# Performance work log

Measured on AMD Instinct MI355X. Metric: run time of the kernel, lower is better.

Reference implementation:

```python
import jax, jax.numpy as jnp
import numpy as np

N_HEAD = 8
DQK = 64
DV = 64
D_IN = 512
D_OUT = 512
D_MID = 2048
B = 4
L = 2048
EPS = 1e-5


def layernorm(x):
    mu = jnp.mean(x, axis=-1, keepdims=True)
    var = jnp.mean(jnp.square(x - mu), axis=-1, keepdims=True)
    return (x - mu) / jnp.sqrt(var + EPS)


def setup_inputs() -> dict:
    key = jax.random.key(0)
    ks = jax.random.split(key, 10)
    s = 0.02
    return {
        "query": jax.random.normal(ks[0], (B, L, D_IN), jnp.float32),
        "key": jax.random.normal(ks[1], (B, L, D_IN), jnp.float32),
        "value": jax.random.normal(ks[2], (B, L, D_IN), jnp.float32),
        "mask": jnp.zeros((B, L, L), jnp.float32),
        "WQ": jax.random.normal(ks[3], (D_IN, N_HEAD * DQK), jnp.float32) * s,
        "WK": jax.random.normal(ks[4], (D_IN, N_HEAD * DQK), jnp.float32) * s,
        "WV": jax.random.normal(ks[5], (D_IN, N_HEAD * DV), jnp.float32) * s,
        "WO": jax.random.normal(ks[6], (N_HEAD * DV, D_OUT), jnp.float32) * s,
        "W1": jax.random.normal(ks[7], (D_OUT, D_MID), jnp.float32) * s,
        "W2": jax.random.normal(ks[8], (D_MID, D_OUT), jnp.float32) * s,
    }


def reference(query, key, value, mask, WQ, WK, WV, WO, W1, W2):
    bsz = query.shape[0]
    # projections -> [b, h, l, d]
    Q = (query @ WQ).reshape(bsz, -1, N_HEAD, DQK).transpose(0, 2, 1, 3)
    K = (key @ WK).reshape(bsz, -1, N_HEAD, DQK).transpose(0, 2, 1, 3)
    V = (value @ WV).reshape(bsz, -1, N_HEAD, DV).transpose(0, 2, 1, 3)
    # scaled dot-product attention with additive mask [b, 1, lq, lk]
    scores = jnp.einsum("bhqd,bhkd->bhqk", Q, K) / jnp.sqrt(jnp.float32(DQK))
    w = jax.nn.softmax(scores + mask[:, None, :, :], axis=-1)
    out = jnp.einsum("bhqk,bhkd->bhqd", w, V)
    out = out.transpose(0, 2, 1, 3).reshape(bsz, -1, N_HEAD * DV)
    out = out @ WO
    out = layernorm(query + out)
    ff = jax.nn.relu(out @ W1) @ W2
    return layernorm(out + ff)
```

## Files before the change

### kernel.cpp

```cpp
#include <hip/hip_runtime.h>
#include <hip/hip_bf16.h>

using bf16 = __bf16;
typedef __bf16 bf16x4 __attribute__((ext_vector_type(4)));
typedef __bf16 bf16x8 __attribute__((ext_vector_type(8)));
typedef float f32x4 __attribute__((ext_vector_type(4)));

static constexpr int BATCH = 4;
static constexpr int SEQ   = 2048;
static constexpr int DIN   = 512;
static constexpr int NHEAD = 8;
static constexpr int DMID  = 2048;
static constexpr int MROWS = BATCH * SEQ;

__global__ __launch_bounds__(256) void mask_check(const uint4* __restrict__ m,
                                                  int* __restrict__ flag)
{
    const int base = (blockIdx.x * 256 + threadIdx.x) * 4;
    unsigned nz = 0;
    for (int i = 0; i < 4; ++i) {
        const uint4 v = m[base + i];
        nz |= v.x | v.y | v.z | v.w;
    }
    if (nz) atomicOr(flag, 1);
}

__global__ __launch_bounds__(256) void transpose_weights(
    const float* __restrict__ WQ, const float* __restrict__ WK,
    const float* __restrict__ WV, const float* __restrict__ WO,
    const float* __restrict__ W1, const float* __restrict__ W2,
    bf16* __restrict__ WQt, bf16* __restrict__ WKt, bf16* __restrict__ WVt,
    bf16* __restrict__ WOt, bf16* __restrict__ W1t, bf16* __restrict__ W2t)
{
    __shared__ float tile[32][33];
    const int bid = blockIdx.x;
    const float* in; bf16* out; int ip, op, cx, ry;
    if (bid < 1024) {
        const int w = bid >> 8, idx = bid & 255;
        in  = w == 0 ? WQ  : w == 1 ? WK  : w == 2 ? WV  : WO;
        out = w == 0 ? WQt : w == 1 ? WKt : w == 2 ? WVt : WOt;
        ip = 512; op = 512; cx = idx & 15; ry = idx >> 4;
    } else if (bid < 2048) {
        const int idx = bid - 1024;
        in = W1; out = W1t; ip = 2048; op = 512; cx = idx & 63; ry = idx >> 6;
    } else {
        const int idx = bid - 2048;
        in = W2; out = W2t; ip = 512; op = 2048; cx = idx & 15; ry = idx >> 4;
    }
    const int c0 = cx * 32, r0 = ry * 32;
    const int tx = threadIdx.x & 31, ty = threadIdx.x >> 5;
    for (int i = 0; i < 32; i += 8)
        tile[ty + i][tx] = in[(size_t)(r0 + ty + i) * ip + c0 + tx];
    __syncthreads();
    for (int i = 0; i < 32; i += 8)
        out[(size_t)(c0 + ty + i) * op + r0 + tx] = (bf16)tile[tx][ty + i];
}

__global__ __launch_bounds__(256) void transpose_b2b(const bf16* __restrict__ in,
                                                     bf16* __restrict__ out,
                                                     int ip, int op)
{
    __shared__ bf16 tile[32][33];
    const int c0 = blockIdx.x * 32;
    const int r0 = blockIdx.y * 32;
    const int tx = threadIdx.x & 31;
    const int ty = threadIdx.x >> 5;
    for (int i = 0; i < 32; i += 8)
        tile[ty + i][tx] = in[(size_t)(r0 + ty + i) * ip + c0 + tx];
    __syncthreads();
    for (int i = 0; i < 32; i += 8)
        out[(size_t)(c0 + ty + i) * op + r0 + tx] = tile[tx][ty + i];
}

template <int ACT>
__global__ __launch_bounds__(256) void gemm_skinny(const bf16* __restrict__ A,
                                                   const bf16* __restrict__ Bt,
                                                   bf16* __restrict__ C,
                                                   int M, int N, int K)
{
    __shared__ bf16 sA[32 * 72];
    __shared__ bf16 sB[256 * 72];

    const int t    = threadIdx.x;
    const int lane = t & 63;
    const int wave = t >> 6;
    const int wm   = wave >> 1;
    const int wn   = wave & 1;
    const int lr   = lane & 15;
    const int lq   = lane >> 4;

    const int m0 = blockIdx.y * 32;
    const int n0 = blockIdx.x * 256;

    const int ar = t >> 3;
    const int ac = (t & 7) * 8;

    f32x4 acc[8] = {};

    for (int k0 = 0; k0 < K; k0 += 64) {
        int4 av = *reinterpret_cast<const int4*>(A + (size_t)(m0 + ar) * K + k0 + ac);
        int4 bv[8];
        for (int i = 0; i < 8; ++i)
            bv[i] = *reinterpret_cast<const int4*>(Bt + (size_t)(n0 + i * 32 + ar) * K + k0 + ac);

        *reinterpret_cast<int4*>(&sA[ar * 72 + ac]) = av;
        for (int i = 0; i < 8; ++i)
            *reinterpret_cast<int4*>(&sB[(i * 32 + ar) * 72 + ac]) = bv[i];
        __syncthreads();

        for (int kk = 0; kk < 2; ++kk) {
            bf16x8 af = *reinterpret_cast<const bf16x8*>(&sA[(wm * 16 + lr) * 72 + kk * 32 + lq * 8]);
            for (int ni = 0; ni < 8; ++ni) {
                bf16x8 bfr = *reinterpret_cast<const bf16x8*>(&sB[(wn * 128 + ni * 16 + lr) * 72 + kk * 32 + lq * 8]);
                acc[ni] = __builtin_amdgcn_mfma_f32_16x16x32_bf16(af, bfr, acc[ni], 0, 0, 0);
            }
        }
        __syncthreads();
    }

    for (int ni = 0; ni < 8; ++ni) {
        const int col = n0 + wn * 128 + ni * 16 + lr;
        for (int j = 0; j < 4; ++j) {
            const int row = m0 + wm * 16 + lq * 4 + j;
            float v = acc[ni][j];
            if (ACT == 1) v = v > 0.f ? v : 0.f;
            C[(size_t)row * N + col] = (bf16)v;
        }
    }
}

__device__ inline int4 cvt16(const float* p)
{
    const float4 f0 = *reinterpret_cast<const float4*>(p);
    const float4 f1 = *reinterpret_cast<const float4*>(p + 4);
    bf16x8 r;
    r[0] = (bf16)f0.x; r[1] = (bf16)f0.y; r[2] = (bf16)f0.z; r[3] = (bf16)f0.w;
    r[4] = (bf16)f1.x; r[5] = (bf16)f1.y; r[6] = (bf16)f1.z; r[7] = (bf16)f1.w;
    return *reinterpret_cast<int4*>(&r);
}

__global__ __launch_bounds__(256) void gemm_qkv(const float* __restrict__ q,
                                                const float* __restrict__ k,
                                                const float* __restrict__ v,
                                                const bf16* __restrict__ WQt,
                                                const bf16* __restrict__ WKt,
                                                const bf16* __restrict__ WVt,
                                                bf16* __restrict__ Qb,
                                                bf16* __restrict__ Kb,
                                                bf16* __restrict__ Vb)
{
    const float* A  = blockIdx.z == 0 ? q   : blockIdx.z == 1 ? k   : v;
    const bf16*  Bt = blockIdx.z == 0 ? WQt : blockIdx.z == 1 ? WKt : WVt;
    bf16*        C  = blockIdx.z == 0 ? Qb  : blockIdx.z == 1 ? Kb  : Vb;
    const int K = DIN, N = DIN;

    __shared__ bf16 sA[32 * 72];
    __shared__ bf16 sB[256 * 72];

    const int t    = threadIdx.x;
    const int lane = t & 63;
    const int wave = t >> 6;
    const int wm   = wave >> 1;
    const int wn   = wave & 1;
    const int lr   = lane & 15;
    const int lq   = lane >> 4;

    const int m0 = blockIdx.y * 32;
    const int n0 = blockIdx.x * 256;

    const int ar = t >> 3;
    const int ac = (t & 7) * 8;

    f32x4 acc[8] = {};

    for (int k0 = 0; k0 < K; k0 += 64) {
        int4 av = cvt16(A + (size_t)(m0 + ar) * K + k0 + ac);
        int4 bv[8];
        for (int i = 0; i < 8; ++i)
            bv[i] = *reinterpret_cast<const int4*>(Bt + (size_t)(n0 + i * 32 + ar) * K + k0 + ac);

        *reinterpret_cast<int4*>(&sA[ar * 72 + ac]) = av;
        for (int i = 0; i < 8; ++i)
            *reinterpret_cast<int4*>(&sB[(i * 32 + ar) * 72 + ac]) = bv[i];
        __syncthreads();

        for (int kk = 0; kk < 2; ++kk) {
            bf16x8 af = *reinterpret_cast<const bf16x8*>(&sA[(wm * 16 + lr) * 72 + kk * 32 + lq * 8]);
            for (int ni = 0; ni < 8; ++ni) {
                bf16x8 bfr = *reinterpret_cast<const bf16x8*>(&sB[(wn * 128 + ni * 16 + lr) * 72 + kk * 32 + lq * 8]);
                acc[ni] = __builtin_amdgcn_mfma_f32_16x16x32_bf16(af, bfr, acc[ni], 0, 0, 0);
            }
        }
        __syncthreads();
    }

    for (int ni = 0; ni < 8; ++ni) {
        const int col = n0 + wn * 128 + ni * 16 + lr;
        for (int j = 0; j < 4; ++j) {
            const int row = m0 + wm * 16 + lq * 4 + j;
            C[(size_t)row * N + col] = (bf16)acc[ni][j];
        }
    }
}

__global__ __launch_bounds__(256) void attn_kernel(const bf16* __restrict__ Qb,
                                                   const bf16* __restrict__ Kb,
                                                   const bf16* __restrict__ Vt,
                                                   const float* __restrict__ mask,
                                                   bf16* __restrict__ O,
                                                   const int* __restrict__ mzf)
{
    const int bi   = blockIdx.x;
    const int xcd  = bi & 7;
    const int slot = bi >> 3;
    const int pair = xcd * 4 + (slot >> 5);
    const int qt   = slot & 31;
    const int h    = pair >> 2;
    const int b    = pair & 3;

    const int t    = threadIdx.x;
    const int lane = t & 63;
    const int wave = t >> 6;
    const int lr   = lane & 15;
    const int lq   = lane >> 4;
    const int q0   = qt * 64;
    const bool useM = (*mzf != 0);

    __shared__ bf16 sK[64 * 72];
    __shared__ bf16 sV[64 * 72];
    __shared__ bf16 sP[4][16 * 72];
    __shared__ bf16 sM[64 * 68];

    const int  qrow = q0 + wave * 16 + lr;
    const bf16* qp  = Qb + (size_t)(b * SEQ + qrow) * DIN + h * 64 + lq * 8;
    const bf16x8 qf0 = *reinterpret_cast<const bf16x8*>(qp);
    const bf16x8 qf1 = *reinterpret_cast<const bf16x8*>(qp + 32);

    f32x4 o[4] = {};
    f32x4 lrow = {};

    const int sr = t >> 2;
    const int sc = (t & 3) << 3;

    const bf16*  kbase = Kb + (size_t)(b * SEQ) * DIN + h * 64;
    const bf16*  vbase = Vt + (size_t)(h * 64 + sr) * MROWS + b * SEQ;
    const float* mbase = mask + ((size_t)b * SEQ + q0) * SEQ;

    constexpr float L2E = 1.4426950408889634f;
    constexpr float SCL = 0.125f * L2E;
    const bf16x8 ones = {(bf16)1.f, (bf16)1.f, (bf16)1.f, (bf16)1.f,
                         (bf16)1.f, (bf16)1.f, (bf16)1.f, (bf16)1.f};

    int4 kr0 = *reinterpret_cast<const int4*>(kbase + (size_t)sr * DIN + sc);
    int4 kr1 = *reinterpret_cast<const int4*>(kbase + (size_t)sr * DIN + sc + 32);
    int4 vr0 = *reinterpret_cast<const int4*>(vbase + sc);
    int4 vr1 = *reinterpret_cast<const int4*>(vbase + sc + 32);

    for (int tile = 0; tile < SEQ / 64; ++tile) {
        if (tile) __syncthreads();

        *reinterpret_cast<int4*>(&sK[sr * 72 + sc])      = kr0;
        *reinterpret_cast<int4*>(&sK[sr * 72 + sc + 32]) = kr1;
        *reinterpret_cast<int4*>(&sV[sr * 72 + sc])      = vr0;
        *reinterpret_cast<int4*>(&sV[sr * 72 + sc + 32]) = vr1;
        if (useM) {
            const int k0 = tile * 64;
            for (int i = 0; i < 4; ++i) {
                const int idx = t + 256 * i;
                const float4 mr = *reinterpret_cast<const float4*>(
                    mbase + (size_t)(idx >> 4) * SEQ + k0 + (idx & 15) * 4);
                bf16x4 mv;
                mv[0] = (bf16)(mr.x * L2E); mv[1] = (bf16)(mr.y * L2E);
                mv[2] = (bf16)(mr.z * L2E); mv[3] = (bf16)(mr.w * L2E);
                *reinterpret_cast<bf16x4*>(&sM[(idx >> 4) * 68 + (idx & 15) * 4]) = mv;
            }
        }

        if (tile + 1 < SEQ / 64) {
            const int k0 = (tile + 1) * 64;
            kr0 = *reinterpret_cast<const int4*>(kbase + (size_t)(k0 + sr) * DIN + sc);
            kr1 = *reinterpret_cast<const int4*>(kbase + (size_t)(k0 + sr) * DIN + sc + 32);
            vr0 = *reinterpret_cast<const int4*>(vbase + k0 + sc);
            vr1 = *reinterpret_cast<const int4*>(vbase + k0 + sc + 32);
        }
        __syncthreads();

        f32x4 sf[4] = {};
        for (int s = 0; s < 2; ++s) {
            const bf16x8 qf = s ? qf1 : qf0;
            for (int ni = 0; ni < 4; ++ni) {
                bf16x8 kf = *reinterpret_cast<const bf16x8*>(&sK[(ni * 16 + lr) * 72 + s * 32 + lq * 8]);
                sf[ni] = __builtin_amdgcn_mfma_f32_16x16x32_bf16(qf, kf, sf[ni], 0, 0, 0);
            }
        }

        if (useM) {
            for (int j = 0; j < 4; ++j) {
                const int mr2 = (wave * 16 + lq * 4 + j) * 68;
                for (int ni = 0; ni < 4; ++ni) {
                    const float mval = (float)sM[mr2 + ni * 16 + lr];
                    sP[wave][(lq * 4 + j) * 72 + ni * 16 + lr] = (bf16)exp2f(sf[ni][j] * SCL + mval);
                }
            }
        } else {
            for (int j = 0; j < 4; ++j)
                for (int ni = 0; ni < 4; ++ni)
                    sP[wave][(lq * 4 + j) * 72 + ni * 16 + lr] = (bf16)exp2f(sf[ni][j] * SCL);
        }

        f32x4 rs = {};
        for (int s = 0; s < 2; ++s) {
            bf16x8 pf = *reinterpret_cast<const bf16x8*>(&sP[wave][lr * 72 + s * 32 + lq * 8]);
            rs = __builtin_amdgcn_mfma_f32_16x16x32_bf16(pf, ones, rs, 0, 0, 0);
            for (int ni = 0; ni < 4; ++ni) {
                bf16x8 vf = *reinterpret_cast<const bf16x8*>(&sV[(ni * 16 + lr) * 72 + s * 32 + lq * 8]);
                o[ni] = __builtin_amdgcn_mfma_f32_16x16x32_bf16(pf, vf, o[ni], 0, 0, 0);
            }
        }
        for (int j = 0; j < 4; ++j)
            lrow[j] += rs[j];
    }

    for (int ni = 0; ni < 4; ++ni)
        for (int j = 0; j < 4; ++j) {
            const int row = q0 + wave * 16 + lq * 4 + j;
            const int col = h * 64 + ni * 16 + lr;
            O[(size_t)(b * SEQ + row) * DIN + col] = (bf16)(o[ni][j] / lrow[j]);
        }
}

__global__ __launch_bounds__(256) void add_ln(const float* __restrict__ X,
                                              const bf16* __restrict__ Y,
                                              bf16* __restrict__ Ob,
                                              float* __restrict__ Of)
{
    const int row  = blockIdx.x * 4 + (threadIdx.x >> 6);
    const int lane = threadIdx.x & 63;
    const size_t base = (size_t)row * DIN + lane * 8;
    const float4 x0 = *reinterpret_cast<const float4*>(X + base);
    const float4 x1 = *reinterpret_cast<const float4*>(X + base + 4);
    const bf16x8 yv = *reinterpret_cast<const bf16x8*>(Y + base);
    float v[8] = {x0.x, x0.y, x0.z, x0.w, x1.x, x1.y, x1.z, x1.w};
    float s = 0.f;
    for (int i = 0; i < 8; ++i) { v[i] += (float)yv[i]; s += v[i]; }
    for (int off = 1; off < 64; off <<= 1) s += __shfl_xor(s, off);
    const float mu = s * (1.f / DIN);
    float var = 0.f;
    for (int i = 0; i < 8; ++i) { const float d = v[i] - mu; var += d * d; }
    for (int off = 1; off < 64; off <<= 1) var += __shfl_xor(var, off);
    const float rstd = rsqrtf(var * (1.f / DIN) + 1e-5f);
    float r[8];
    for (int i = 0; i < 8; ++i) r[i] = (v[i] - mu) * rstd;
    if (Ob) {
        bf16x8 ov;
        for (int i = 0; i < 8; ++i) ov[i] = (bf16)r[i];
        *reinterpret_cast<bf16x8*>(Ob + base) = ov;
    }
    if (Of) {
        *reinterpret_cast<float4*>(Of + base)     = make_float4(r[0], r[1], r[2], r[3]);
        *reinterpret_cast<float4*>(Of + base + 4) = make_float4(r[4], r[5], r[6], r[7]);
    }
}

extern "C" void kernel_launch(void* const* d_in, const int* in_sizes, int n_in,
                              void* d_out, int out_size, void* d_ws, size_t ws_size,
                              hipStream_t stream)
{
    const float* query = (const float*)d_in[0];
    const float* key   = (const float*)d_in[1];
    const float* value = (const float*)d_in[2];
    const float* mask  = (const float*)d_in[3];
    const float* WQ    = (const float*)d_in[4];
    const float* WK    = (const float*)d_in[5];
    const float* WV    = (const float*)d_in[6];
    const float* WO    = (const float*)d_in[7];
    const float* W1    = (const float*)d_in[8];
    const float* W2    = (const float*)d_in[9];

    char* w = (char*)d_ws;
    size_t off = 0;
    auto carve2 = [&](size_t elems) { bf16* p = (bf16*)(w + off); off += elems * 2; return p; };
    auto carve4 = [&](size_t elems) { float* p = (float*)(w + off); off += elems * 4; return p; };

    bf16* Qb    = carve2((size_t)MROWS * DIN);
    bf16* Kb    = carve2((size_t)MROWS * DIN);
    bf16* Vb    = carve2((size_t)MROWS * DIN);
    bf16* Vt    = carve2((size_t)MROWS * DIN);
    bf16* Mid   = carve2((size_t)MROWS * DMID);
    float* Ln1f = carve4((size_t)MROWS * DIN);
    bf16* WQt   = carve2((size_t)DIN * DIN);
    bf16* WKt   = carve2((size_t)DIN * DIN);
    bf16* WVt   = carve2((size_t)DIN * DIN);
    bf16* WOt   = carve2((size_t)DIN * DIN);
    bf16* W1t   = carve2((size_t)DIN * DMID);
    bf16* W2t   = carve2((size_t)DMID * DIN);
    int*  mzf   = (int*)(w + off); off += 16;
    if (off > ws_size) return;

    bf16* Ob   = Vb;
    bf16* Two  = Qb;
    bf16* Ln1b = Kb;
    bf16* F2   = Vt;

    const dim3 blk(256);

    hipMemsetAsync(mzf, 0, 4, stream);
    mask_check<<<dim3(4096), blk, 0, stream>>>((const uint4*)mask, mzf);

    transpose_weights<<<dim3(3072), blk, 0, stream>>>(WQ, WK, WV, WO, W1, W2,
                                                      WQt, WKt, WVt, WOt, W1t, W2t);

    gemm_qkv<<<dim3(DIN / 256, MROWS / 32, 3), blk, 0, stream>>>(query, key, value,
                                                                 WQt, WKt, WVt, Qb, Kb, Vb);

    transpose_b2b<<<dim3(DIN / 32, MROWS / 32), blk, 0, stream>>>(Vb, Vt, DIN, MROWS);

    attn_kernel<<<dim3(1024), blk, 0, stream>>>(Qb, Kb, Vt, mask, Ob, mzf);

    gemm_skinny<0><<<dim3(DIN / 256, MROWS / 32), blk, 0, stream>>>(Ob, WOt, Two, MROWS, DIN, DIN);
    add_ln<<<dim3(MROWS / 4), blk, 0, stream>>>(query, Two, Ln1b, Ln1f);

    gemm_skinny<1><<<dim3(DMID / 256, MROWS / 32), blk, 0, stream>>>(Ln1b, W1t, Mid, MROWS, DMID, DIN);
    gemm_skinny<0><<<dim3(DIN / 256, MROWS / 32), blk, 0, stream>>>(Mid, W2t, F2, MROWS, DIN, DMID);

    add_ln<<<dim3(MROWS / 4), blk, 0, stream>>>(Ln1f, F2, (bf16*)nullptr, (float*)d_out);
}
```

Before: 393.9 us.

## Switch GEMMs to 128x128 tiles with direct global-to-LDS loads

Replaces the 32x256 skinny GEMM tiles with square 128x128 tiles. Each wave now computes a 4x4 grid of 16x16 MFMA outputs, which raises operand reuse from shared memory and cuts global traffic per FLOP. The bf16 operand loads use the global_load_lds builtin to write straight into LDS, bypassing registers. The fp32 QKV input path still converts through registers. The LDS rows lose their padding, which may add bank conflicts on fragment reads, and there is no double buffering.

```diff
diff --git a/kernel.cpp b/kernel.cpp
--- a/kernel.cpp
+++ b/kernel.cpp
@@ -12,6 +12,13 @@
 static constexpr int NHEAD = 8;
 static constexpr int DMID  = 2048;
 static constexpr int MROWS = BATCH * SEQ;
+
+__device__ __forceinline__ void gload16(const void* g, void* l)
+{
+    __builtin_amdgcn_global_load_lds(
+        (const __attribute__((address_space(1))) unsigned int*)g,
+        (__attribute__((address_space(3))) unsigned int*)l, 16, 0, 0);
+}
 
 __global__ __launch_bounds__(256) void mask_check(const uint4* __restrict__ m,
                                                   int* __restrict__ flag)
@@ -72,15 +79,13 @@
         out[(size_t)(c0 + ty + i) * op + r0 + tx] = tile[tx][ty + i];
 }
 
-template <int ACT>
-__global__ __launch_bounds__(256) void gemm_skinny(const bf16* __restrict__ A,
-                                                   const bf16* __restrict__ Bt,
-                                                   bf16* __restrict__ C,
-                                                   int M, int N, int K)
-{
-    __shared__ bf16 sA[32 * 72];
-    __shared__ bf16 sB[256 * 72];
-
+template <int ACT, bool AF32>
+__device__ __forceinline__ void gemm128_body(const void* __restrict__ Ain,
+                                             const bf16* __restrict__ Bt,
+                                             bf16* __restrict__ C,
+                                             int N, int K,
+                                             bf16* sA, bf16* sB)
+{
     const int t    = threadIdx.x;
     const int lane = t & 63;
     const int wave = t >> 6;
@@ -89,118 +94,111 @@
     const int lr   = lane & 15;
     const int lq   = lane >> 4;
 
-    const int m0 = blockIdx.y * 32;
-    const int n0 = blockIdx.x * 256;
-
-    const int ar = t >> 3;
-    const int ac = (t & 7) * 8;
-
-    f32x4 acc[8] = {};
+    const int m0 = blockIdx.y * 128;
+    const int n0 = blockIdx.x * 128;
+
+    const int srow = lane >> 3;
+    const int scol = (lane & 7) * 8;
+
+    f32x4 acc[4][4] = {};
 
     for (int k0 = 0; k0 < K; k0 += 64) {
-        int4 av = *reinterpret_cast<const int4*>(A + (size_t)(m0 + ar) * K + k0 + ac);
-        int4 bv[8];
-        for (int i = 0; i < 8; ++i)
-            bv[i] = *reinterpret_cast<const int4*>(Bt + (size_t)(n0 + i * 32 + ar) * K + k0 + ac);
-
-        *reinterpret_cast<int4*>(&sA[ar * 72 + ac]) = av;
-        for (int i = 0; i < 8; ++i)
-            *reinterpret_cast<int4*>(&sB[(i * 32 + ar) * 72 + ac]) = bv[i];
+        if constexpr (AF32) {
+            const float* Af = (const float*)Ain;
+            float4 fa[8];
+#pragma unroll
+            for (int i = 0; i < 4; ++i) {
+                const float* p = Af + (size_t)(m0 + (wave * 4 + i) * 8 + srow) * K + k0 + scol;
+                fa[2 * i]     = *reinterpret_cast<const float4*>(p);
+                fa[2 * i + 1] = *reinterpret_cast<const float4*>(p + 4);
+            }
+            if (k0) __syncthreads();
+#pragma unroll
+            for (int i = 0; i < 4; ++i) {
+                const int ch = wave * 4 + i;
+                gload16(Bt + (size_t)(n0 + ch * 8 + srow) * K + k0 + scol, sB + ch * 512);
+            }
+#pragma unroll
+            for (int i = 0; i < 4; ++i) {
+                const int r = (wave * 4 + i) * 8 + srow;
+                const float4 a = fa[2 * i], b = fa[2 * i + 1];
+                bf16x8 h;
+                h[0] = (bf16)a.x; h[1] = (bf16)a.y; h[2] = (bf16)a.z; h[3] = (bf16)a.w;
+                h[4] = (bf16)b.x; h[5] = (bf16)b.y; h[6] = (bf16)b.z; h[7] = (bf16)b.w;
+                *reinterpret_cast<bf16x8*>(&sA[r * 64 + scol]) = h;
+            }
+        } else {
+            const bf16* Ab = (const bf16*)Ain;
+            if (k0) __syncthreads();
+#pragma unroll
+            for (int i = 0; i < 4; ++i) {
+                const int ch = wave * 4 + i;
+                const int r  = ch * 8 + srow;
+                gload16(Ab + (size_t)(m0 + r) * K + k0 + scol, sA + ch * 512);
+                gload16(Bt + (size_t)(n0 + r) * K + k0 + scol, sB + ch * 512);
+            }
+        }
         __syncthreads();
 
+#pragma unroll
         for (int kk = 0; kk < 2; ++kk) {
-            bf16x8 af = *reinterpret_cast<const bf16x8*>(&sA[(wm * 16 + lr) * 72 + kk * 32 + lq * 8]);
-            for (int ni = 0; ni < 8; ++ni) {
-                bf16x8 bfr = *reinterpret_cast<const bf16x8*>(&sB[(wn * 128 + ni * 16 + lr) * 72 + kk * 32 + lq * 8]);
-                acc[ni] = __builtin_amdgcn_mfma_f32_16x16x32_bf16(af, bfr, acc[ni], 0, 0, 0);
-            }
-        }
-        __syncthreads();
-    }
-
-    for (int ni = 0; ni < 8; ++ni) {
-        const int col = n0 + wn * 128 + ni * 16 + lr;
-        for (int j = 0; j < 4; ++j) {
-            const int row = m0 + wm * 16 + lq * 4 + j;
-            float v = acc[ni][j];
-            if (ACT == 1) v = v > 0.f ? v : 0.f;
-            C[(size_t)row * N + col] = (bf16)v;
-        }
-    }
-}
-
-__device__ inline int4 cvt16(const float* p)
-{
-    const float4 f0 = *reinterpret_cast<const float4*>(p);
-    const float4 f1 = *reinterpret_cast<const float4*>(p + 4);
-    bf16x8 r;
-    r[0] = (bf16)f0.x; r[1] = (bf16)f0.y; r[2] = (bf16)f0.z; r[3] = (bf16)f0.w;
-    r[4] = (bf16)f1.x; r[5] = (bf16)f1.y; r[6] = (bf16)f1.z; r[7] = (bf16)f1.w;
-    return *reinterpret_cast<int4*>(&r);
-}
-
-__global__ __launch_bounds__(256) void gemm_qkv(const float* __restrict__ q,
-                                                const float* __restrict__ k,
-                                                const float* __restrict__ v,
-                                                const bf16* __restrict__ WQt,
-                                                const bf16* __restrict__ WKt,
-                                                const bf16* __restrict__ WVt,
-                                                bf16* __restrict__ Qb,
-                                                bf16* __restrict__ Kb,
-                                                bf16* __restrict__ Vb)
-{
-    const float* A  = blockIdx.z == 0 ? q   : blockIdx.z == 1 ? k   : v;
-    const bf16*  Bt = blockIdx.z == 0 ? WQt : blockIdx.z == 1 ? WKt : WVt;
-    bf16*        C  = blockIdx.z == 0 ? Qb  : blockIdx.z == 1 ? Kb  : Vb;
-    const int K = DIN, N = DIN;
-
-    __shared__ bf16 sA[32 * 72];
-    __shared__ bf16 sB[256 * 72];
-
-    const int t    = threadIdx.x;
-    const int lane = t & 63;
-    const int wave = t >> 6;
-    const int wm   = wave >> 1;
-    const int wn   = wave & 1;
-    const int lr   = lane & 15;
-    const int lq   = lane >> 4;
-
-    const int m0 = blockIdx.y * 32;
-    const int n0 = blockIdx.x * 256;
-
-    const int ar = t >> 3;
-    const int ac = (t & 7) * 8;
-
-    f32x4 acc[8] = {};
-
-    for (int k0 = 0; k0 < K; k0 += 64) {
-        int4 av = cvt16(A + (size_t)(m0 + ar) * K + k0 + ac);
-        int4 bv[8];
-        for (int i = 0; i < 8; ++i)
-            bv[i] = *reinterpret_cast<const int4*>(Bt + (size_t)(n0 + i * 32 + ar) * K + k0 + ac);
-
-        *reinterpret_cast<int4*>(&sA[ar * 72 + ac]) = av;
-        for (int i = 0; i < 8; ++i)
-            *reinterpret_cast<int4*>(&sB[(i * 32 + ar) * 72 + ac]) = bv[i];
-        __syncthreads();
-
-        for (int kk = 0; kk < 2; ++kk) {
-            bf16x8 af = *reinterpret_cast<const bf16x8*>(&sA[(wm * 16 + lr) * 72 + kk * 32 + lq * 8]);
-            for (int ni = 0; ni < 8; ++ni) {
-                bf16x8 bfr = *reinterpret_cast<const bf16x8*>(&sB[(wn * 128 + ni * 16 + lr) * 72 + kk * 32 + lq * 8]);
-                acc[ni] = __builtin_amdgcn_mfma_f32_16x16x32_bf16(af, bfr, acc[ni], 0, 0, 0);
-            }
-        }
-        __syncthreads();
-    }
-
-    for (int ni = 0; ni < 8; ++ni) {
-        const int col = n0 + wn * 128 + ni * 16 + lr;
-        for (int j = 0; j < 4; ++j) {
-            const int row = m0 + wm * 16 + lq * 4 + j;
-            C[(size_t)row * N + col] = (bf16)acc[ni][j];
-        }
-    }
+            bf16x8 af[4], bfr[4];
+#pragma unroll
+            for (int x = 0; x < 4; ++x) {
+                af[x]  = *reinterpret_cast<const bf16x8*>(&sA[(wm * 64 + x * 16 + lr) * 64 + kk * 32 + lq * 8]);
+                bfr[x] = *reinterpret_cast<const bf16x8*>(&sB[(wn * 64 + x * 16 + lr) * 64 + kk * 32 + lq * 8]);
+            }
+#pragma unroll
+            for (int m = 0; m < 4; ++m)
+#pragma unroll
+                for (int n = 0; n < 4; ++n)
+                    acc[m][n] = __builtin_amdgcn_mfma_f32_16x16x32_bf16(af[m], bfr[n], acc[m][n], 0, 0, 0);
+        }
+    }
+
+#pragma unroll
+    for (int n = 0; n < 4; ++n) {
+        const int col = n0 + wn * 64 + n * 16 + lr;
+#pragma unroll
+        for (int m = 0; m < 4; ++m) {
+            const int rowb = m0 + wm * 64 + m * 16 + lq * 4;
+#pragma unroll
+            for (int j = 0; j < 4; ++j) {
+                float v = acc[m][n][j];
+                if (ACT == 1) v = v > 0.f ? v : 0.f;
+                C[(size_t)(rowb + j) * N + col] = (bf16)v;
+            }
+        }
+    }
+}
+
+template <int ACT>
+__global__ __launch_bounds__(256) void gemm128(const bf16* __restrict__ A,
+                                               const bf16* __restrict__ Bt,
+                                               bf16* __restrict__ C,
+                                               int N, int K)
+{
+    __shared__ bf16 sA[128 * 64];
+    __shared__ bf16 sB[128 * 64];
+    gemm128_body<ACT, false>(A, Bt, C, N, K, sA, sB);
+}
+
+__global__ __launch_bounds__(256) void gemm128_qkv(const float* __restrict__ q,
+                                                   const float* __restrict__ k,
+                                                   const float* __restrict__ v,
+                                                   const bf16* __restrict__ WQt,
+                                                   const bf16* __restrict__ WKt,
+                                                   const bf16* __restrict__ WVt,
+                                                   bf16* __restrict__ Qb,
+                                                   bf16* __restrict__ Kb,
+                                                   bf16* __restrict__ Vb)
+{
+    __shared__ bf16 sA[128 * 64];
+    __shared__ bf16 sB[128 * 64];
+    const void* A  = blockIdx.z == 0 ? (const void*)q : blockIdx.z == 1 ? (const void*)k : (const void*)v;
+    const bf16* Bt = blockIdx.z == 0 ? WQt : blockIdx.z == 1 ? WKt : WVt;
+    bf16*       C  = blockIdx.z == 0 ? Qb  : blockIdx.z == 1 ? Kb  : Vb;
+    gemm128_body<0, true>(A, Bt, C, DIN, DIN, sA, sB);
 }
 
 __global__ __launch_bounds__(256) void attn_kernel(const bf16* __restrict__ Qb,
@@ -410,18 +408,18 @@
     transpose_weights<<<dim3(3072), blk, 0, stream>>>(WQ, WK, WV, WO, W1, W2,
                                                       WQt, WKt, WVt, WOt, W1t, W2t);
 
-    gemm_qkv<<<dim3(DIN / 256, MROWS / 32, 3), blk, 0, stream>>>(query, key, value,
-                                                                 WQt, WKt, WVt, Qb, Kb, Vb);
+    gemm128_qkv<<<dim3(DIN / 128, MROWS / 128, 3), blk, 0, stream>>>(query, key, value,
+                                                                     WQt, WKt, WVt, Qb, Kb, Vb);
 
     transpose_b2b<<<dim3(DIN / 32, MROWS / 32), blk, 0, stream>>>(Vb, Vt, DIN, MROWS);
 
     attn_kernel<<<dim3(1024), blk, 0, stream>>>(Qb, Kb, Vt, mask, Ob, mzf);
 
-    gemm_skinny<0><<<dim3(DIN / 256, MROWS / 32), blk, 0, stream>>>(Ob, WOt, Two, MROWS, DIN, DIN);
+    gemm128<0><<<dim3(DIN / 128, MROWS / 128), blk, 0, stream>>>(Ob, WOt, Two, DIN, DIN);
     add_ln<<<dim3(MROWS / 4), blk, 0, stream>>>(query, Two, Ln1b, Ln1f);
 
-    gemm_skinny<1><<<dim3(DMID / 256, MROWS / 32), blk, 0, stream>>>(Ln1b, W1t, Mid, MROWS, DMID, DIN);
-    gemm_skinny<0><<<dim3(DIN / 256, MROWS / 32), blk, 0, stream>>>(Mid, W2t, F2, MROWS, DIN, DMID);
+    gemm128<1><<<dim3(DMID / 128, MROWS / 128), blk, 0, stream>>>(Ln1b, W1t, Mid, DMID, DIN);
+    gemm128<0><<<dim3(DIN / 128, MROWS / 128), blk, 0, stream>>>(Mid, W2t, F2, DIN, DMID);
 
     add_ln<<<dim3(MROWS / 4), blk, 0, stream>>>(Ln1f, F2, (bf16*)nullptr, (float*)d_out);
 }
```

Measured after the change: 372.7 us. -5.4%, faster.
